# Performance work log

Measured on AMD Instinct MI355X. Metric: run time of the kernel, lower is better.

## Reference

```python
import jax, jax.numpy as jnp
import numpy as np

NEUMANN_TERMS = 6
EPS_PASSTHROUGH = 1e-6  # hn_config.GRADIENT_PASSTHROUGH_EPSILON (assumed)


def _cayley_neumann(W, terms=NEUMANN_TERMS):
    """Cayley transform U = (I - A)^{-1} (I + A) with A = skew(W),
    where (I - A)^{-1} is approximated by the truncated Neumann series
    sum_{k=0}^{terms-1} A^k."""
    A = 0.5 * (W - W.T)                       # skew-symmetric generator
    I = jnp.eye(W.shape[0], dtype=W.dtype)
    S = I
    P = I
    for _ in range(terms - 1):                # small fixed loop (neumann_terms)
        P = P @ A
        S = S + P
    return S @ (I + A)


def _quantum_rotation(h, theta):
    """Parametric quantum rotation activation: rotate adjacent feature pairs
    by angle theta (norm-preserving, replaces ReLU/GELU)."""
    N, d = h.shape
    hp = h.reshape(N, d // 2, 2)
    c, s = jnp.cos(theta), jnp.sin(theta)
    x0, x1 = hp[..., 0], hp[..., 1]
    r0 = c * x0 - s * x1
    r1 = s * x0 + c * x1
    return jnp.stack([r0, r1], axis=-1).reshape(N, d)


def setup_inputs() -> dict:
    key = jax.random.key(0)
    k1, k2, k3 = jax.random.split(key, 3)
    N, d_model, d_ff = 65536, 1024, 1024
    inputs = jax.random.normal(k1, (N, d_model), dtype=jnp.float32)
    # Orthogonal initializer with gain 0.1 (as in build())
    q1 = jnp.linalg.qr(jax.random.normal(k2, (d_ff, d_model), dtype=jnp.float32))[0]
    q2 = jnp.linalg.qr(jax.random.normal(k3, (d_model, d_ff), dtype=jnp.float32))[0]
    u1_weights = 0.1 * q1
    u2_weights = 0.1 * q2
    activation_angle = jnp.float32(0.7854)  # pi/4 initializer
    return {"inputs": inputs, "u1_weights": u1_weights,
            "u2_weights": u2_weights, "activation_angle": activation_angle}


def reference(inputs, u1_weights, u2_weights, activation_angle):
    U1 = _cayley_neumann(u1_weights)          # [d_ff, d_model]
    U2 = _cayley_neumann(u2_weights)          # [d_model, d_ff]
    h = inputs @ U1.T                         # [N, d_ff]
    h = _quantum_rotation(h, activation_angle)
    out = h @ U2.T                            # [N, d_model]
    # gradient passthrough term from call()
    passthrough = (jnp.mean(u1_weights) * EPS_PASSTHROUGH
                   + jnp.mean(u2_weights) * EPS_PASSTHROUGH
                   + activation_angle * EPS_PASSTHROUGH)
    return out + passthrough
```

## Files before the change

### kernel.cpp

```cpp
#include <hip/hip_runtime.h>
#include <hip/hip_bf16.h>
#include <stdint.h>


#define MM (1024 * 1024)

typedef __attribute__((ext_vector_type(4))) float f32x4;
typedef __attribute__((ext_vector_type(8))) short bf16x8;

__device__ __forceinline__ ushort f2bf(float f) {
  uint32_t u = __builtin_bit_cast(uint32_t, f);
  u += 0x7FFFu + ((u >> 16) & 1u);
  return (ushort)(u >> 16);
}
__device__ __forceinline__ float bf2f(ushort h) {
  uint32_t u = ((uint32_t)h) << 16;
  return __builtin_bit_cast(float, u);
}

__device__ __forceinline__ void gld_lds16(const ushort* g, ushort* l) {
  __builtin_amdgcn_global_load_lds(
      (const __attribute__((address_space(1))) unsigned int*)g,
      (__attribute__((address_space(3))) unsigned int*)l, 16, 0, 0);
}

__global__ __launch_bounds__(256, 2) void gemm_bt(
    const ushort* __restrict__ X0, const ushort* __restrict__ X1,
    const ushort* __restrict__ Y0, const ushort* __restrict__ Y1,
    float* __restrict__ o32, ushort* __restrict__ o16,
    int M, int N, int K, int mode,
    const float* __restrict__ theta_p, const float* __restrict__ sums) {
  __shared__ ushort lA[128 * 32];
  __shared__ ushort lB[128 * 32];

  const int tid = threadIdx.x;
  const int wave = tid >> 6, lane = tid & 63;
  const int bn = blockIdx.x, bm = blockIdx.y, bz = blockIdx.z;
  const int job = bz >> 1, mi = bz & 1;

  const ushort* X = (job ? X1 : X0) + (size_t)mi * MM;
  const ushort* Y = (job ? Y1 : Y0) + (size_t)mi * MM;

  const ushort* Xg = X + (size_t)(bm * 128 + (tid >> 2)) * K + (tid & 3) * 8;
  const ushort* Yg = Y + (size_t)(bn * 128 + (tid >> 2)) * K + (tid & 3) * 8;
  ushort* lAw = lA + wave * 512;
  ushort* lBw = lB + wave * 512;

  const int wm = (wave & 1) * 64;
  const int wn = (wave >> 1) * 64;
  const int lr = lane & 15;
  const int kq = (lane >> 4) * 8;

  f32x4 acc[4][4] = {};

  for (int k0 = 0; k0 < K; k0 += 32) {
    __syncthreads();
    gld_lds16(Xg + k0, lAw);
    gld_lds16(Xg + k0 + (size_t)64 * K, lAw + 64 * 32);
    gld_lds16(Yg + k0, lBw);
    gld_lds16(Yg + k0 + (size_t)64 * K, lBw + 64 * 32);
    __syncthreads();

    bf16x8 af[4], bfg[4];
#pragma unroll
    for (int t = 0; t < 4; ++t) {
      af[t] = *(const bf16x8*)(lA + (wm + t * 16 + lr) * 32 + kq);
      bfg[t] = *(const bf16x8*)(lB + (wn + t * 16 + lr) * 32 + kq);
    }
#pragma unroll
    for (int ti = 0; ti < 4; ++ti)
#pragma unroll
      for (int tj = 0; tj < 4; ++tj)
        acc[ti][tj] = __builtin_amdgcn_mfma_f32_16x16x32_bf16(
            af[ti], bfg[tj], acc[ti][tj], 0, 0, 0);
  }

  const int q4 = (lane >> 4) * 4;
  if (mode == 0) {
    float* O = o32 + (size_t)bz * MM;
#pragma unroll
    for (int ti = 0; ti < 4; ++ti)
#pragma unroll
      for (int r = 0; r < 4; ++r) {
        size_t row = (size_t)(bm * 128 + wm + ti * 16 + q4 + r);
        float* Orow = O + row * N;
#pragma unroll
        for (int tj = 0; tj < 4; ++tj)
          Orow[bn * 128 + wn + tj * 16 + lr] = acc[ti][tj][r];
      }
  } else if (mode == 1) {
    float th = *theta_p, s, c;
    __sincosf(th, &s, &c);
    const float ssgn = (lane & 1) ? s : -s;
#pragma unroll
    for (int ti = 0; ti < 4; ++ti)
#pragma unroll
      for (int r = 0; r < 4; ++r) {
        size_t row = (size_t)(bm * 128 + wm + ti * 16 + q4 + r);
        ushort* Orow = o16 + row * N;
#pragma unroll
        for (int tj = 0; tj < 4; ++tj) {
          float v = acc[ti][tj][r];
          float w = __shfl_xor(v, 1);
          Orow[bn * 128 + wn + tj * 16 + lr] = f2bf(c * v + ssgn * w);
        }
      }
  } else {
    const float pt = 1e-6f * (sums[0] * (1.0f / 1048576.0f) +
                              sums[1] * (1.0f / 1048576.0f) + *theta_p);
#pragma unroll
    for (int ti = 0; ti < 4; ++ti)
#pragma unroll
      for (int r = 0; r < 4; ++r) {
        size_t row = (size_t)(bm * 128 + wm + ti * 16 + q4 + r);
        float* Orow = o32 + row * N;
#pragma unroll
        for (int tj = 0; tj < 4; ++tj)
          Orow[bn * 128 + wn + tj * 16 + lr] = acc[ti][tj][r] + pt;
      }
  }
}

__global__ __launch_bounds__(256) void prep_a(const float* __restrict__ W1,
                                              const float* __restrict__ W2,
                                              ushort* __restrict__ Abf,
                                              float* __restrict__ sums) {
  __shared__ float sT[32][33];
  const int z = blockIdx.z;
  const float* W = z ? W2 : W1;
  ushort* A = Abf + (size_t)z * MM;
  const int r0 = blockIdx.y * 32, c0 = blockIdx.x * 32;
  const int x = threadIdx.x, y = threadIdx.y;

#pragma unroll
  for (int k = 0; k < 4; ++k)
    sT[y + 8 * k][x] = W[(size_t)(c0 + y + 8 * k) * 1024 + r0 + x];
  __syncthreads();

  float lsum = 0.f;
#pragma unroll
  for (int k = 0; k < 4; ++k) {
    int i = y + 8 * k;
    float w = W[(size_t)(r0 + i) * 1024 + c0 + x];
    lsum += w;
    A[(size_t)(r0 + i) * 1024 + c0 + x] = f2bf(0.5f * (w - sT[x][i]));
  }
#pragma unroll
  for (int off = 32; off > 0; off >>= 1) lsum += __shfl_down(lsum, off);
  if (((y * 32 + x) & 63) == 0) atomicAdd(&sums[z], lsum);
}

__global__ __launch_bounds__(256) void cvt_x(const float* __restrict__ x,
                                             ushort* __restrict__ xb) {
  const size_t i = (size_t)blockIdx.x * 256 + threadIdx.x;
  float4 v = ((const float4*)x)[i];
  ushort4 o;
  o.x = f2bf(v.x);
  o.y = f2bf(v.y);
  o.z = f2bf(v.z);
  o.w = f2bf(v.w);
  ((ushort4*)xb)[i] = o;
}

__global__ __launch_bounds__(256) void ew(const float* __restrict__ S1,
                                          const float* __restrict__ S2,
                                          const float* __restrict__ S3,
                                          const float* __restrict__ S4,
                                          ushort* __restrict__ O0,
                                          ushort* __restrict__ O1, int mode) {
  const int idx = blockIdx.x * 256 + threadIdx.x;
  const int local = idx & (MM - 1);
  const float diag = ((local >> 10) == (local & 1023)) ? 1.f : 0.f;
  if (mode == 0) {
    O0[idx] = f2bf(-S1[idx]);
  } else if (mode == 1) {
    float s2 = S2[idx];
    O0[idx] = f2bf(s2);
    O1[idx] = f2bf(diag - S1[idx] + s2);
  } else {
    O0[idx] =
        f2bf(diag - 2.f * S1[idx] + 2.f * S2[idx] + 2.f * S3[idx] + S4[idx]);
  }
}

extern "C" void kernel_launch(void* const* d_in, const int* in_sizes, int n_in,
                              void* d_out, int out_size, void* d_ws,
                              size_t ws_size, hipStream_t stream) {
  const float* xin = (const float*)d_in[0];
  const float* w1 = (const float*)d_in[1];
  const float* w2 = (const float*)d_in[2];
  const float* th = (const float*)d_in[3];
  float* out = (float*)d_out;

  char* w = (char*)d_ws;
  float* sums = (float*)w;
  ushort* Abf = (ushort*)(w + 256);
  ushort* Bbf = Abf + 2 * MM;
  ushort* B2bf = Bbf + 2 * MM;
  ushort* Fbf = B2bf + 2 * MM;
  ushort* Ubf = Fbf + 2 * MM;
  float* S1 = (float*)(Ubf + 2 * MM);
  float* S2 = S1 + 2 * MM;
  float* S34 = S2 + 2 * MM;
  ushort* xbf = (ushort*)(S34 + 4 * MM);
  ushort* hbf = xbf + (size_t)65536 * 1024;

  hipMemsetAsync(sums, 0, 2 * sizeof(float), stream);

  prep_a<<<dim3(32, 32, 2), dim3(32, 8), 0, stream>>>(w1, w2, Abf, sums);
  cvt_x<<<65536, 256, 0, stream>>>(xin, xbf);

  gemm_bt<<<dim3(8, 8, 2), 256, 0, stream>>>(Abf, Abf, Abf, Abf, S1, nullptr,
                                             1024, 1024, 1024, 0, th, sums);
  ew<<<8192, 256, 0, stream>>>(S1, S2, S34, S34 + 2 * MM, Bbf, nullptr, 0);
  gemm_bt<<<dim3(8, 8, 2), 256, 0, stream>>>(Bbf, Bbf, Bbf, Bbf, S2, nullptr,
                                             1024, 1024, 1024, 0, th, sums);
  ew<<<8192, 256, 0, stream>>>(S1, S2, S34, S34 + 2 * MM, B2bf, Fbf, 1);
  gemm_bt<<<dim3(8, 8, 4), 256, 0, stream>>>(Abf, B2bf, Fbf, Bbf, S34, nullptr,
                                             1024, 1024, 1024, 0, th, sums);
  ew<<<8192, 256, 0, stream>>>(S1, S2, S34, S34 + 2 * MM, Ubf, nullptr, 2);

  gemm_bt<<<dim3(8, 512, 1), 256, 0, stream>>>(xbf, xbf, Ubf, Ubf, nullptr,
                                               hbf, 65536, 1024, 1024, 1, th,
                                               sums);
  gemm_bt<<<dim3(8, 512, 1), 256, 0, stream>>>(hbf, hbf, Ubf + MM, Ubf + MM,
                                               out, nullptr, 65536, 1024, 1024,
                                               2, th, sums);
}
```

Before: 1.007 ms.

## Fuse elementwise prep into GEMM epilogues and swizzle workgroup order

Folds the first two elementwise kernels (negation and the S2/diag-S1+S2 conversions) into the epilogues of the small weight GEMMs through new modes 3 and 4, removing two launches and their extra reads of the fp32 intermediates. It also remaps the linear workgroup index so that consecutive workgroups are spread across row-blocks, which changes the L2/MALL reuse pattern of the large GEMMs. The epilogue adds bf16 stores and one aux read per element, and the swizzle assumes grid x equals 8 and a grid size divisible by 8.

Measured after the change: 972.0 us. 1.04x faster.

```diff
diff --git a/kernel.cpp b/kernel.cpp
--- a/kernel.cpp
+++ b/kernel.cpp
@@ -28,6 +28,7 @@
     const ushort* __restrict__ X0, const ushort* __restrict__ X1,
     const ushort* __restrict__ Y0, const ushort* __restrict__ Y1,
     float* __restrict__ o32, ushort* __restrict__ o16,
+    ushort* __restrict__ o16b, const float* __restrict__ aux,
     int M, int N, int K, int mode,
     const float* __restrict__ theta_p, const float* __restrict__ sums) {
   __shared__ ushort lA[128 * 32];
@@ -35,8 +36,14 @@
 
   const int tid = threadIdx.x;
   const int wave = tid >> 6, lane = tid & 63;
-  const int bn = blockIdx.x, bm = blockIdx.y, bz = blockIdx.z;
+  const int bz = blockIdx.z;
   const int job = bz >> 1, mi = bz & 1;
+
+  const int nwg = gridDim.x * gridDim.y;
+  const int lin = blockIdx.y * gridDim.x + blockIdx.x;
+  const int swz = (lin & 7) * (nwg >> 3) + (lin >> 3);
+  const int bn = swz & 7;
+  const int bm = swz >> 3;
 
   const ushort* X = (job ? X1 : X0) + (size_t)mi * MM;
   const ushort* Y = (job ? Y1 : Y0) + (size_t)mi * MM;
@@ -76,19 +83,7 @@
   }
 
   const int q4 = (lane >> 4) * 4;
-  if (mode == 0) {
-    float* O = o32 + (size_t)bz * MM;
-#pragma unroll
-    for (int ti = 0; ti < 4; ++ti)
-#pragma unroll
-      for (int r = 0; r < 4; ++r) {
-        size_t row = (size_t)(bm * 128 + wm + ti * 16 + q4 + r);
-        float* Orow = O + row * N;
-#pragma unroll
-        for (int tj = 0; tj < 4; ++tj)
-          Orow[bn * 128 + wn + tj * 16 + lr] = acc[ti][tj][r];
-      }
-  } else if (mode == 1) {
+  if (mode == 1) {
     float th = *theta_p, s, c;
     __sincosf(th, &s, &c);
     const float ssgn = (lane & 1) ? s : -s;
@@ -105,7 +100,7 @@
           Orow[bn * 128 + wn + tj * 16 + lr] = f2bf(c * v + ssgn * w);
         }
       }
-  } else {
+  } else if (mode == 2) {
     const float pt = 1e-6f * (sums[0] * (1.0f / 1048576.0f) +
                               sums[1] * (1.0f / 1048576.0f) + *theta_p);
 #pragma unroll
@@ -117,6 +112,31 @@
 #pragma unroll
         for (int tj = 0; tj < 4; ++tj)
           Orow[bn * 128 + wn + tj * 16 + lr] = acc[ti][tj][r] + pt;
+      }
+  } else {
+    float* O = o32 + (size_t)bz * MM;
+    ushort* P0 = (mode >= 3) ? o16 + (size_t)bz * MM : nullptr;
+    ushort* P1 = (mode == 4) ? o16b + (size_t)bz * MM : nullptr;
+    const float* Ax = (mode == 4) ? aux + (size_t)bz * MM : nullptr;
+#pragma unroll
+    for (int ti = 0; ti < 4; ++ti)
+#pragma unroll
+      for (int r = 0; r < 4; ++r) {
+        const int row = bm * 128 + wm + ti * 16 + q4 + r;
+        const size_t base = (size_t)row * N;
+#pragma unroll
+        for (int tj = 0; tj < 4; ++tj) {
+          const int col = bn * 128 + wn + tj * 16 + lr;
+          const float v = acc[ti][tj][r];
+          O[base + col] = v;
+          if (mode == 3) {
+            P0[base + col] = f2bf(-v);
+          } else if (mode == 4) {
+            P0[base + col] = f2bf(v);
+            const float diag = (row == col) ? 1.f : 0.f;
+            P1[base + col] = f2bf(diag - Ax[base + col] + v);
+          }
+        }
       }
   }
 }
@@ -166,21 +186,12 @@
                                           const float* __restrict__ S2,
                                           const float* __restrict__ S3,
                                           const float* __restrict__ S4,
-                                          ushort* __restrict__ O0,
-                                          ushort* __restrict__ O1, int mode) {
+                                          ushort* __restrict__ O0) {
   const int idx = blockIdx.x * 256 + threadIdx.x;
   const int local = idx & (MM - 1);
   const float diag = ((local >> 10) == (local & 1023)) ? 1.f : 0.f;
-  if (mode == 0) {
-    O0[idx] = f2bf(-S1[idx]);
-  } else if (mode == 1) {
-    float s2 = S2[idx];
-    O0[idx] = f2bf(s2);
-    O1[idx] = f2bf(diag - S1[idx] + s2);
-  } else {
-    O0[idx] =
-        f2bf(diag - 2.f * S1[idx] + 2.f * S2[idx] + 2.f * S3[idx] + S4[idx]);
-  }
+  O0[idx] =
+      f2bf(diag - 2.f * S1[idx] + 2.f * S2[idx] + 2.f * S3[idx] + S4[idx]);
 }
 
 extern "C" void kernel_launch(void* const* d_in, const int* in_sizes, int n_in,
@@ -210,20 +221,21 @@
   prep_a<<<dim3(32, 32, 2), dim3(32, 8), 0, stream>>>(w1, w2, Abf, sums);
   cvt_x<<<65536, 256, 0, stream>>>(xin, xbf);
 
-  gemm_bt<<<dim3(8, 8, 2), 256, 0, stream>>>(Abf, Abf, Abf, Abf, S1, nullptr,
-                                             1024, 1024, 1024, 0, th, sums);
-  ew<<<8192, 256, 0, stream>>>(S1, S2, S34, S34 + 2 * MM, Bbf, nullptr, 0);
-  gemm_bt<<<dim3(8, 8, 2), 256, 0, stream>>>(Bbf, Bbf, Bbf, Bbf, S2, nullptr,
-                                             1024, 1024, 1024, 0, th, sums);
-  ew<<<8192, 256, 0, stream>>>(S1, S2, S34, S34 + 2 * MM, B2bf, Fbf, 1);
+  gemm_bt<<<dim3(8, 8, 2), 256, 0, stream>>>(Abf, Abf, Abf, Abf, S1, Bbf,
+                                             nullptr, nullptr, 1024, 1024,
+                                             1024, 3, th, sums);
+  gemm_bt<<<dim3(8, 8, 2), 256, 0, stream>>>(Bbf, Bbf, Bbf, Bbf, S2, B2bf,
+                                             Fbf, S1, 1024, 1024, 1024, 4, th,
+                                             sums);
   gemm_bt<<<dim3(8, 8, 4), 256, 0, stream>>>(Abf, B2bf, Fbf, Bbf, S34, nullptr,
-                                             1024, 1024, 1024, 0, th, sums);
-  ew<<<8192, 256, 0, stream>>>(S1, S2, S34, S34 + 2 * MM, Ubf, nullptr, 2);
+                                             nullptr, nullptr, 1024, 1024,
+                                             1024, 0, th, sums);
+  ew<<<8192, 256, 0, stream>>>(S1, S2, S34, S34 + 2 * MM, Ubf);
 
   gemm_bt<<<dim3(8, 512, 1), 256, 0, stream>>>(xbf, xbf, Ubf, Ubf, nullptr,
-                                               hbf, 65536, 1024, 1024, 1, th,
-                                               sums);
+                                               hbf, nullptr, nullptr, 65536,
+                                               1024, 1024, 1, th, sums);
   gemm_bt<<<dim3(8, 512, 1), 256, 0, stream>>>(hbf, hbf, Ubf + MM, Ubf + MM,
-                                               out, nullptr, 65536, 1024, 1024,
-                                               2, th, sums);
-}
+                                               out, nullptr, nullptr, nullptr,
+                                               65536, 1024, 1024, 2, th, sums);
+}
```
